# Optimization experiments

Hardware: AMD Instinct MI355X
Metric: run time of the kernel (lower is better)

Reference implementation:

```python
import jax, jax.numpy as jnp
import numpy as np

B, T, V, E, H, C = 128, 200, 50000, 300, 512, 3

def _lstm_scan(x, W_ih, W_hh, b_ih, b_hh, h0, c0):
    # x: [B,T,E]; torch LSTMCell gate order: i, f, g, o
    xg = jnp.einsum('bte,ge->btg', x, W_ih) + b_ih + b_hh  # [B,T,4H]
    def step(carry, xg_t):
        h, c = carry
        gates = xg_t + h @ W_hh.T
        i, f, g, o = jnp.split(gates, 4, axis=-1)
        c = jax.nn.sigmoid(f) * c + jax.nn.sigmoid(i) * jnp.tanh(g)
        h = jax.nn.sigmoid(o) * jnp.tanh(c)
        return (h, c), (h, c)
    _, (hs, cs) = jax.lax.scan(step, (h0, c0), jnp.swapaxes(xg, 0, 1))
    return hs, cs  # [T,B,H]

def _mask_blend(hs, cs, m, h0, c0):
    # hs,cs: [T,B,H]; m: [T,B]; carry-forward previous state where mask==0
    def step(carry, inp):
        h_p, c_p = carry
        h_t, c_t, m_t = inp
        m_t = m_t[:, None]
        h_p = m_t * h_t + (1.0 - m_t) * h_p
        c_p = m_t * c_t + (1.0 - m_t) * c_p
        return (h_p, c_p), (h_p, c_p)
    _, (mh, mc) = jax.lax.scan(step, (h0, c0), (hs, cs, m))
    return mh, mc

def setup_inputs() -> dict:
    key = jax.random.key(0)
    ks = jax.random.split(key, 12)
    s_e = 1.0 / np.sqrt(H)
    u = lambda k, shp: jax.random.uniform(k, shp, jnp.float32, -s_e, s_e)
    return {
        'premise': jax.random.randint(ks[0], (B, T), 0, V),
        'hypothesis': jax.random.randint(ks[1], (B, T), 0, V),
        'similarity': jax.random.uniform(ks[2], (B, 1), jnp.float32),
        'emb_weight': jax.random.normal(ks[3], (V, E), jnp.float32),
        'Wih_p': u(ks[4], (4 * H, E)), 'Whh_p': u(ks[5], (4 * H, H)),
        'bih_p': u(ks[6], (4 * H,)), 'bhh_p': u(ks[7], (4 * H,)),
        'Wih_h': u(ks[8], (4 * H, E)), 'Whh_h': u(ks[9], (4 * H, H)),
        'bih_h': u(ks[10], (4 * H,)), 'bhh_h': u(ks[11], (4 * H,)),
        'fc_W': jax.random.normal(jax.random.fold_in(key, 100), (C, H + 1), jnp.float32) * 0.02,
        'fc_b': jnp.zeros((C,), jnp.float32),
    }

def reference(premise, hypothesis, similarity, emb_weight,
              Wih_p, Whh_p, bih_p, bhh_p, Wih_h, Whh_h, bih_h, bhh_h,
              fc_W, fc_b):
    emb_p = emb_weight[premise]            # [B,T,E]
    emb_h = emb_weight[hypothesis]
    mask_p = (premise != 0).astype(jnp.float32).T   # [T,B]
    mask_h = (hypothesis != 0).astype(jnp.float32).T
    h0 = jnp.zeros((B, H), jnp.float32)
    c0 = jnp.zeros((B, H), jnp.float32)
    # premise LSTM (raw, unmasked recurrence as in original)
    hs_p, cs_p = _lstm_scan(emb_p, Wih_p, Whh_p, bih_p, bhh_p, h0, c0)
    _, mc_p = _mask_blend(hs_p, cs_p, mask_p, h0, c0)
    c_last = mc_p[-1]                      # masked last premise cell
    # hypothesis LSTM: hidden reset, cell carried
    hs_h, cs_h = _lstm_scan(emb_h, Wih_h, Whh_h, bih_h, bhh_h, h0, c_last)
    mh_h, _ = _mask_blend(hs_h, cs_h, mask_h, h0, c_last)
    feat = jnp.concatenate([mh_h[-1], similarity], axis=1)  # [B,H+1]
    logits = feat @ fc_W.T + fc_b
    # dropout inactive (eval mode)
    return jax.nn.log_softmax(logits, axis=1)
```

## Files before the change

kernel.cpp:

```cpp
#include <hip/hip_runtime.h>
#include <hip/hip_bf16.h>

#define B_ 128
#define T_ 200
#define H_ 512
#define G_ 2048
#define E_ 300

typedef unsigned short u16;
typedef unsigned int u32;

using f32x4 = __attribute__((ext_vector_type(4))) float;
using s16x8 = __attribute__((ext_vector_type(8))) short;
using u32x2 = __attribute__((ext_vector_type(2))) u32;

__device__ __forceinline__ u16 f2bf(float f) {
  u32 u = __builtin_bit_cast(u32, f);
  u32 r = (u + 0x7fffu + ((u >> 16) & 1u)) >> 16;
  return (u16)r;
}
__device__ __forceinline__ float bf2f(u16 s) {
  return __builtin_bit_cast(float, (u32)s << 16);
}

__device__ __forceinline__ s16x8 ld_h16_sc(const void* p) {
  s16x8 r;
  asm volatile("global_load_dwordx4 %0, %1, off sc0 sc1" : "=v"(r) : "v"(p));
  return r;
}
__device__ __forceinline__ void st_h_sc(void* p, u32 v) {
  asm volatile("global_store_short %0, %1, off sc0 sc1" :: "v"(p), "v"(v));
}
__device__ __forceinline__ u32 ld_flag_sc(const void* p) {
  u32 r;
  asm volatile("global_load_dword %0, %1, off sc0 sc1\n\ts_waitcnt vmcnt(0)"
               : "=v"(r) : "v"(p) : "memory");
  return r;
}
__device__ __forceinline__ void st_flag_sc(void* p, u32 v) {
  asm volatile("global_store_dword %0, %1, off sc0 sc1" :: "v"(p), "v"(v) : "memory");
}

__global__ __launch_bounds__(256) void wih_cvt(
    const float* __restrict__ W, u16* __restrict__ Wb)
{
  const int idx = blockIdx.x * 256 + threadIdx.x;
  const int row = idx / 320, k = idx - row * 320;
  const float v = (k < E_) ? W[row * E_ + k] : 0.f;
  Wb[idx] = f2bf(v);
}

__global__ __launch_bounds__(64) void mask_k(
    const int* __restrict__ tok, u32* __restrict__ mb)
{
  const int idx = blockIdx.x * 64 + threadIdx.x;
  if (idx >= T_ * 4) return;
  const int t = idx >> 2, w = idx & 3;
  u32 bits = 0;
  for (int i = 0; i < 32; ++i)
    bits |= (tok[(w * 32 + i) * T_ + t] != 0 ? 1u : 0u) << i;
  mb[idx] = bits;
}

__global__ __launch_bounds__(256) void xg_gemm(
    const int* __restrict__ tok, const float* __restrict__ emb,
    const u16* __restrict__ Wb, const float* __restrict__ bih,
    const float* __restrict__ bhh, u16* __restrict__ xg)
{
  __shared__ u16 Al[64 * 320];
  __shared__ u16 Bl[32 * 320];
  __shared__ int tks[64];
  const int tid = threadIdx.x;
  const int bx = blockIdx.x;
  const int m0 = bx * 64;
  if (tid < 64) tks[tid] = tok[((bx & 1) * 64 + tid) * T_ + (bx >> 1)];
  __syncthreads();
  {
    const int row = tid >> 2, part = tid & 3;
    const float* erow = emb + (size_t)tks[row] * E_;
    char* base = (char*)Al + row * 640;
    const int swz = (row & 7) << 4;
#pragma unroll
    for (int i = 0; i < 40; ++i) {
      const int kw = part * 40 + i;
      const int k = kw * 2;
      const float v0 = (k < E_) ? erow[k] : 0.f;
      const float v1 = (k + 1 < E_) ? erow[k + 1] : 0.f;
      *(u32*)(base + ((kw * 4) ^ swz)) = (u32)f2bf(v0) | ((u32)f2bf(v1) << 16);
    }
  }
  __syncthreads();
  const int wv = tid >> 6, ln = tid & 63, lr = ln & 15, lq = ln >> 4;
  const int arow = wv * 16 + lr;
  const char* abase = (const char*)Al + arow * 640;
  const int aswz = (arow & 7) << 4;
  const int brow = tid >> 3, bpart = tid & 7;
  char* bdst = (char*)Bl + brow * 640;
  const int bswz = (brow & 7) << 4;
  const char* b0base = (const char*)Bl + lr * 640;
  const char* b1base = (const char*)Bl + (16 + lr) * 640;
  const int bswz2 = (lr & 7) << 4;

  for (int ni = 0; ni < 8; ++ni) {
    const int n0 = blockIdx.y * 256 + ni * 32;
    {
      const u16* src = Wb + (size_t)(n0 + brow) * 320 + bpart * 40;
#pragma unroll
      for (int i = 0; i < 5; ++i) {
        s16x8 v = *(const s16x8*)(src + i * 8);
        *(s16x8*)(bdst + (((bpart * 5 + i) * 16) ^ bswz)) = v;
      }
    }
    __syncthreads();
    f32x4 acc0 = {0.f, 0.f, 0.f, 0.f}, acc1 = {0.f, 0.f, 0.f, 0.f};
#pragma unroll
    for (int ks = 0; ks < 10; ++ks) {
      const int kb = ks * 64 + lq * 16;
      s16x8 af  = *(const s16x8*)(abase  + (kb ^ aswz));
      s16x8 bf0 = *(const s16x8*)(b0base + (kb ^ bswz2));
      s16x8 bf1 = *(const s16x8*)(b1base + (kb ^ bswz2));
      acc0 = __builtin_amdgcn_mfma_f32_16x16x32_bf16(af, bf0, acc0, 0, 0, 0);
      acc1 = __builtin_amdgcn_mfma_f32_16x16x32_bf16(af, bf1, acc1, 0, 0, 0);
    }
    const int qc = n0 >> 9;
    const int jA = (n0 & 511) + lr;
#pragma unroll
    for (int r = 0; r < 4; ++r) {
      const int m = m0 + wv * 16 + lq * 4 + r;
      const int gA = n0 + lr, gB = n0 + 16 + lr;
      xg[(size_t)m * 2048 + (size_t)jA * 4 + qc]        = f2bf(acc0[r] + bih[gA] + bhh[gA]);
      xg[(size_t)m * 2048 + (size_t)(jA + 16) * 4 + qc] = f2bf(acc1[r] + bih[gB] + bhh[gB]);
    }
    __syncthreads();
  }
}

template<int TRACK_C>
__global__ __launch_bounds__(512, 2) void lstm_rec(
    const u16* __restrict__ xg, const float* __restrict__ Whh,
    u16* __restrict__ hbuf, const float* __restrict__ c0in,
    float* __restrict__ cOut, float* __restrict__ mhOut,
    u32* __restrict__ flags, const u32* __restrict__ maskb)
{
  __shared__ f32x4 red[8][4][64];
  const int tid = threadIdx.x;
  const int wv = tid >> 6, ln = tid & 63, lr = ln & 15, lq = ln >> 4;
  const int grp = (int)blockIdx.x >> 5, jt = (int)blockIdx.x & 31;
  const int j0 = jt * 16, bg0 = grp * 16;
  u32* gflags = flags + grp * 512;

  s16x8 Bf[4][2];
#pragma unroll
  for (int q = 0; q < 4; ++q) {
    const float* wr = Whh + (size_t)(q * H_ + j0 + lr) * H_ + wv * 64 + lq * 8;
#pragma unroll
    for (int ks = 0; ks < 2; ++ks) {
      const float* wp = wr + ks * 32;
      s16x8 f;
#pragma unroll
      for (int i = 0; i < 8; ++i) f[i] = (short)f2bf(wp[i]);
      Bf[q][ks] = f;
    }
  }

  float c[4], mb[4];
#pragma unroll
  for (int r = 0; r < 4; ++r) {
    const int b = bg0 + lq * 4 + r;
    float cv = 0.f;
    if (!TRACK_C && wv == 0) cv = c0in[b * H_ + j0 + lr];
    c[r] = cv;
    mb[r] = TRACK_C ? cv : 0.f;
  }

  const u32* pp = gflags + (ln & 31) * 16;
  const int mword = grp >> 1, mshift = (grp & 1) * 16;

  for (int t = 0; t < T_; ++t) {
    const u16* hrd = hbuf + (t & 1) * (B_ * H_);
    u16* hwr = hbuf + ((t + 1) & 1) * (B_ * H_);

    u32x2 gxp[4];
    u32 mku = 0;
    if (wv == 0) {
      mku = maskb[t * 4 + mword] >> mshift;
#pragma unroll
      for (int r = 0; r < 4; ++r) {
        const int b = bg0 + lq * 4 + r;
        gxp[r] = *(const u32x2*)(xg + (size_t)(t * 128 + b) * 2048
                                    + (size_t)(j0 + lr) * 4);
      }
      if (t > 0) {
        int guard = 0;
        for (;;) {
          u32 v = ld_flag_sc(pp);
          if (__all((int)(v >= (u32)t))) break;
          if (++guard > (1 << 22)) break;
          __builtin_amdgcn_s_sleep(1);
        }
      }
    }
    __syncthreads();
    __builtin_amdgcn_sched_barrier(0);

    s16x8 ha[2];
    const u16* hb = hrd + (size_t)(bg0 + lr) * H_ + wv * 64 + lq * 8;
    ha[0] = ld_h16_sc(hb);
    ha[1] = ld_h16_sc(hb + 32);
    asm volatile("s_waitcnt vmcnt(0)" ::: "memory");
    __builtin_amdgcn_sched_barrier(0);

    f32x4 acc[4];
#pragma unroll
    for (int q = 0; q < 4; ++q) acc[q] = (f32x4){0.f, 0.f, 0.f, 0.f};
#pragma unroll
    for (int ks = 0; ks < 2; ++ks)
#pragma unroll
      for (int q = 0; q < 4; ++q)
        acc[q] = __builtin_amdgcn_mfma_f32_16x16x32_bf16(ha[ks], Bf[q][ks], acc[q], 0, 0, 0);

    if (wv > 0) {
#pragma unroll
      for (int q = 0; q < 4; ++q) red[wv][q][ln] = acc[q];
    }
    __syncthreads();
    if (wv == 0) {
#pragma unroll
      for (int kv = 1; kv < 8; ++kv)
#pragma unroll
        for (int q = 0; q < 4; ++q) acc[q] += red[kv][q][ln];
      const bool last = (t == T_ - 1);
#pragma unroll
      for (int r = 0; r < 4; ++r) {
        const int b = bg0 + lq * 4 + r;
        const u32 lo = gxp[r][0], hi = gxp[r][1];
        const float gi = acc[0][r] + bf2f((u16)lo);
        const float gf = acc[1][r] + bf2f((u16)(lo >> 16));
        const float gG = acc[2][r] + bf2f((u16)hi);
        const float go = acc[3][r] + bf2f((u16)(hi >> 16));
        const float si = 1.f / (1.f + __expf(-gi));
        const float sf = 1.f / (1.f + __expf(-gf));
        const float so = 1.f / (1.f + __expf(-go));
        const float tg = 2.f / (1.f + __expf(-2.f * gG)) - 1.f;
        const float cn = sf * c[r] + si * tg;
        const float tc = 2.f / (1.f + __expf(-2.f * cn)) - 1.f;
        const float hn = so * tc;
        c[r] = cn;
        if ((mku >> (lq * 4 + r)) & 1u) mb[r] = TRACK_C ? cn : hn;
        if (!last) st_h_sc(hwr + (size_t)b * H_ + j0 + lr, (u32)f2bf(hn));
      }
      if (t + 1 < T_) {
        asm volatile("s_waitcnt vmcnt(0)" ::: "memory");
        if (ln == 0) st_flag_sc(gflags + jt * 16, (u32)(t + 1));
      }
    }
    __syncthreads();
  }

  if (wv == 0) {
#pragma unroll
    for (int r = 0; r < 4; ++r) {
      const int b = bg0 + lq * 4 + r;
      if (TRACK_C) cOut[b * H_ + j0 + lr] = mb[r];
      else         mhOut[b * H_ + j0 + lr] = mb[r];
    }
  }
}

__global__ __launch_bounds__(128) void final_k(
    const float* __restrict__ mh, const float* __restrict__ sim,
    const float* __restrict__ fcW, const float* __restrict__ fcb,
    float* __restrict__ out)
{
  const int b = threadIdx.x;
  float l[3];
#pragma unroll
  for (int cc = 0; cc < 3; ++cc) {
    const float* wr = fcW + cc * (H_ + 1);
    float s = fcb[cc] + sim[b] * wr[H_];
    for (int j = 0; j < H_; ++j) s += mh[b * H_ + j] * wr[j];
    l[cc] = s;
  }
  const float m = fmaxf(l[0], fmaxf(l[1], l[2]));
  const float lse = m + logf(__expf(l[0] - m) + __expf(l[1] - m) + __expf(l[2] - m));
  out[b * 3 + 0] = l[0] - lse;
  out[b * 3 + 1] = l[1] - lse;
  out[b * 3 + 2] = l[2] - lse;
}

extern "C" void kernel_launch(void* const* d_in, const int* in_sizes, int n_in,
                              void* d_out, int out_size, void* d_ws, size_t ws_size,
                              hipStream_t stream) {
  const int*   prem = (const int*)d_in[0];
  const int*   hypo = (const int*)d_in[1];
  const float* sim  = (const float*)d_in[2];
  const float* emb  = (const float*)d_in[3];
  const float* WihP = (const float*)d_in[4];
  const float* WhhP = (const float*)d_in[5];
  const float* bihP = (const float*)d_in[6];
  const float* bhhP = (const float*)d_in[7];
  const float* WihH = (const float*)d_in[8];
  const float* WhhH = (const float*)d_in[9];
  const float* bihH = (const float*)d_in[10];
  const float* bhhH = (const float*)d_in[11];
  const float* fcW  = (const float*)d_in[12];
  const float* fcb  = (const float*)d_in[13];
  float* out = (float*)d_out;

  char* ws = (char*)d_ws;
  const size_t XG_BYTES = (size_t)B_ * T_ * G_ * 2;
  const size_t HB_OFF = XG_BYTES;
  const size_t CL_OFF = HB_OFF + (size_t)2 * B_ * H_ * 2;
  const size_t MH_OFF = CL_OFF + (size_t)B_ * H_ * 4;
  const size_t FL_OFF = MH_OFF + (size_t)B_ * H_ * 4;
  const size_t MK_OFF = FL_OFF + 32768;
  const size_t WB_OFF = MK_OFF + 8192;
  const size_t NEED   = WB_OFF + (size_t)G_ * 320 * 2;
  if (ws_size < NEED) return;

  u16*   xg    = (u16*)ws;
  u16*   hbuf  = (u16*)(ws + HB_OFF);
  float* cLast = (float*)(ws + CL_OFF);
  float* mh    = (float*)(ws + MH_OFF);
  u32*   flagsP = (u32*)(ws + FL_OFF);
  u32*   flagsH = flagsP + 4096;
  u32*   maskbP = (u32*)(ws + MK_OFF);
  u32*   maskbH = maskbP + 1024;
  u16*   Wb    = (u16*)(ws + WB_OFF);

  hipMemsetAsync(ws + FL_OFF, 0, 32768, stream);

  dim3 gG(400, 8);
  wih_cvt<<<2560, 256, 0, stream>>>(WihP, Wb);
  mask_k<<<13, 64, 0, stream>>>(prem, maskbP);
  xg_gemm<<<gG, 256, 0, stream>>>(prem, emb, Wb, bihP, bhhP, xg);
  hipMemsetAsync(hbuf, 0, (size_t)B_ * H_ * 2, stream);
  lstm_rec<1><<<256, 512, 0, stream>>>(xg, WhhP, hbuf, nullptr, cLast, nullptr, flagsP, maskbP);
  wih_cvt<<<2560, 256, 0, stream>>>(WihH, Wb);
  mask_k<<<13, 64, 0, stream>>>(hypo, maskbH);
  xg_gemm<<<gG, 256, 0, stream>>>(hypo, emb, Wb, bihH, bhhH, xg);
  hipMemsetAsync(hbuf, 0, (size_t)B_ * H_ * 2, stream);
  lstm_rec<0><<<256, 512, 0, stream>>>(xg, WhhH, hbuf, cLast, nullptr, mh, flagsH, maskbH);
  final_k<<<1, 128, 0, stream>>>(mh, sim, fcW, fcb, out);
}
```

Before: 1.991 ms.

## Replace flag-based inter-block sync with tagged hidden-state words and triple buffering

Removes the per-step global flag barrier between blocks. Each hidden value is now stored as a 32-bit word that packs the bf16 value with a step tag, and consumers poll the h data itself until every tag matches. A triple-buffered h array and a double-buffered LDS reduction allow one __syncthreads per step to be dropped, and the other waves wait on a shared-memory step counter. The trade-off is twice the bytes per h load, extra unpack ALU work, and spin-polling on data that assumes the 32-bit stores are seen atomically.

After: 2.049 ms. 2.9% more time.

```diff
diff --git a/kernel.cpp b/kernel.cpp
--- a/kernel.cpp
+++ b/kernel.cpp
@@ -13,6 +13,7 @@
 using f32x4 = __attribute__((ext_vector_type(4))) float;
 using s16x8 = __attribute__((ext_vector_type(8))) short;
 using u32x2 = __attribute__((ext_vector_type(2))) u32;
+using u32x4 = __attribute__((ext_vector_type(4))) u32;
 
 __device__ __forceinline__ u16 f2bf(float f) {
   u32 u = __builtin_bit_cast(u32, f);
@@ -23,22 +24,13 @@
   return __builtin_bit_cast(float, (u32)s << 16);
 }
 
-__device__ __forceinline__ s16x8 ld_h16_sc(const void* p) {
-  s16x8 r;
+__device__ __forceinline__ u32x4 ld_u32x4_sc(const void* p) {
+  u32x4 r;
   asm volatile("global_load_dwordx4 %0, %1, off sc0 sc1" : "=v"(r) : "v"(p));
   return r;
 }
-__device__ __forceinline__ void st_h_sc(void* p, u32 v) {
-  asm volatile("global_store_short %0, %1, off sc0 sc1" :: "v"(p), "v"(v));
-}
-__device__ __forceinline__ u32 ld_flag_sc(const void* p) {
-  u32 r;
-  asm volatile("global_load_dword %0, %1, off sc0 sc1\n\ts_waitcnt vmcnt(0)"
-               : "=v"(r) : "v"(p) : "memory");
-  return r;
-}
-__device__ __forceinline__ void st_flag_sc(void* p, u32 v) {
-  asm volatile("global_store_dword %0, %1, off sc0 sc1" :: "v"(p), "v"(v) : "memory");
+__device__ __forceinline__ void st_u32_sc(void* p, u32 v) {
+  asm volatile("global_store_dword %0, %1, off sc0 sc1" :: "v"(p), "v"(v));
 }
 
 __global__ __launch_bounds__(256) void wih_cvt(
@@ -138,16 +130,19 @@
 template<int TRACK_C>
 __global__ __launch_bounds__(512, 2) void lstm_rec(
     const u16* __restrict__ xg, const float* __restrict__ Whh,
-    u16* __restrict__ hbuf, const float* __restrict__ c0in,
+    u32* __restrict__ h32, const float* __restrict__ c0in,
     float* __restrict__ cOut, float* __restrict__ mhOut,
-    u32* __restrict__ flags, const u32* __restrict__ maskb)
-{
-  __shared__ f32x4 red[8][4][64];
+    const u32* __restrict__ maskb)
+{
+  __shared__ f32x4 red[2][7][4][64];
+  __shared__ u32 stepS;
   const int tid = threadIdx.x;
   const int wv = tid >> 6, ln = tid & 63, lr = ln & 15, lq = ln >> 4;
   const int grp = (int)blockIdx.x >> 5, jt = (int)blockIdx.x & 31;
   const int j0 = jt * 16, bg0 = grp * 16;
-  u32* gflags = flags + grp * 512;
+  const int BH = B_ * H_;
+  const u32 TAGB = 1u + (TRACK_C ? 0u : 256u);
+  volatile u32* vstep = &stepS;
 
   s16x8 Bf[4][2];
 #pragma unroll
@@ -173,12 +168,21 @@
     mb[r] = TRACK_C ? cv : 0.f;
   }
 
-  const u32* pp = gflags + (ln & 31) * 16;
+  if (wv == 0) {
+#pragma unroll
+    for (int r = 0; r < 4; ++r) {
+      const int b = bg0 + lq * 4 + r;
+      st_u32_sc(h32 + (size_t)b * H_ + j0 + lr, TAGB);
+    }
+  }
+  if (tid == 0) stepS = 0;
+  __syncthreads();
+
   const int mword = grp >> 1, mshift = (grp & 1) * 16;
+  int cur = 0;
 
   for (int t = 0; t < T_; ++t) {
-    const u16* hrd = hbuf + (t & 1) * (B_ * H_);
-    u16* hwr = hbuf + ((t + 1) & 1) * (B_ * H_);
+    const int nxt = (cur == 2) ? 0 : cur + 1;
 
     u32x2 gxp[4];
     u32 mku = 0;
@@ -190,46 +194,67 @@
         gxp[r] = *(const u32x2*)(xg + (size_t)(t * 128 + b) * 2048
                                     + (size_t)(j0 + lr) * 4);
       }
-      if (t > 0) {
-        int guard = 0;
-        for (;;) {
-          u32 v = ld_flag_sc(pp);
-          if (__all((int)(v >= (u32)t))) break;
-          if (++guard > (1 << 22)) break;
-          __builtin_amdgcn_s_sleep(1);
-        }
+    } else {
+      int g0 = 0;
+      while (*vstep < (u32)t) { if (++g0 > (1 << 24)) break; }
+    }
+
+    const u32 tag = TAGB + (u32)t;
+    const u32* hsrc = h32 + (size_t)cur * BH + (size_t)(bg0 + lr) * H_
+                      + wv * 64 + lq * 8;
+    u32x4 hv[4];
+    {
+      int guard = 0;
+      for (;;) {
+        hv[0] = ld_u32x4_sc(hsrc);
+        hv[1] = ld_u32x4_sc(hsrc + 4);
+        hv[2] = ld_u32x4_sc(hsrc + 32);
+        hv[3] = ld_u32x4_sc(hsrc + 36);
+        asm volatile("s_waitcnt vmcnt(0)" ::: "memory");
+        u32 bad = 0;
+#pragma unroll
+        for (int i = 0; i < 4; ++i)
+#pragma unroll
+          for (int e = 0; e < 4; ++e) bad |= (hv[i][e] ^ tag) & 0xFFFFu;
+        if (__all(bad == 0)) break;
+        if (++guard > (1 << 18)) break;
       }
     }
-    __syncthreads();
     __builtin_amdgcn_sched_barrier(0);
 
-    s16x8 ha[2];
-    const u16* hb = hrd + (size_t)(bg0 + lr) * H_ + wv * 64 + lq * 8;
-    ha[0] = ld_h16_sc(hb);
-    ha[1] = ld_h16_sc(hb + 32);
-    asm volatile("s_waitcnt vmcnt(0)" ::: "memory");
-    __builtin_amdgcn_sched_barrier(0);
+    u32x4 w0, w1;
+    w0[0] = (hv[0][0] >> 16) | (hv[0][1] & 0xFFFF0000u);
+    w0[1] = (hv[0][2] >> 16) | (hv[0][3] & 0xFFFF0000u);
+    w0[2] = (hv[1][0] >> 16) | (hv[1][1] & 0xFFFF0000u);
+    w0[3] = (hv[1][2] >> 16) | (hv[1][3] & 0xFFFF0000u);
+    w1[0] = (hv[2][0] >> 16) | (hv[2][1] & 0xFFFF0000u);
+    w1[1] = (hv[2][2] >> 16) | (hv[2][3] & 0xFFFF0000u);
+    w1[2] = (hv[3][0] >> 16) | (hv[3][1] & 0xFFFF0000u);
+    w1[3] = (hv[3][2] >> 16) | (hv[3][3] & 0xFFFF0000u);
+    const s16x8 af0 = __builtin_bit_cast(s16x8, w0);
+    const s16x8 af1 = __builtin_bit_cast(s16x8, w1);
 
     f32x4 acc[4];
 #pragma unroll
-    for (int q = 0; q < 4; ++q) acc[q] = (f32x4){0.f, 0.f, 0.f, 0.f};
-#pragma unroll
-    for (int ks = 0; ks < 2; ++ks)
-#pragma unroll
-      for (int q = 0; q < 4; ++q)
-        acc[q] = __builtin_amdgcn_mfma_f32_16x16x32_bf16(ha[ks], Bf[q][ks], acc[q], 0, 0, 0);
+    for (int q = 0; q < 4; ++q) {
+      acc[q] = __builtin_amdgcn_mfma_f32_16x16x32_bf16(af0, Bf[q][0],
+                   (f32x4){0.f, 0.f, 0.f, 0.f}, 0, 0, 0);
+      acc[q] = __builtin_amdgcn_mfma_f32_16x16x32_bf16(af1, Bf[q][1], acc[q], 0, 0, 0);
+    }
 
     if (wv > 0) {
 #pragma unroll
-      for (int q = 0; q < 4; ++q) red[wv][q][ln] = acc[q];
+      for (int q = 0; q < 4; ++q) red[t & 1][wv - 1][q][ln] = acc[q];
     }
     __syncthreads();
     if (wv == 0) {
 #pragma unroll
       for (int kv = 1; kv < 8; ++kv)
 #pragma unroll
-        for (int q = 0; q < 4; ++q) acc[q] += red[kv][q][ln];
+        for (int q = 0; q < 4; ++q) acc[q] += red[t & 1][kv - 1][q][ln];
       const bool last = (t == T_ - 1);
+      const u32 ntag = TAGB + (u32)(t + 1);
+      u32* hdst = h32 + (size_t)nxt * BH;
 #pragma unroll
       for (int r = 0; r < 4; ++r) {
         const int b = bg0 + lq * 4 + r;
@@ -247,14 +272,13 @@
         const float hn = so * tc;
         c[r] = cn;
         if ((mku >> (lq * 4 + r)) & 1u) mb[r] = TRACK_C ? cn : hn;
-        if (!last) st_h_sc(hwr + (size_t)b * H_ + j0 + lr, (u32)f2bf(hn));
+        if (!last)
+          st_u32_sc(hdst + (size_t)b * H_ + j0 + lr,
+                    ((u32)f2bf(hn) << 16) | ntag);
       }
-      if (t + 1 < T_) {
-        asm volatile("s_waitcnt vmcnt(0)" ::: "memory");
-        if (ln == 0) st_flag_sc(gflags + jt * 16, (u32)(t + 1));
-      }
-    }
-    __syncthreads();
+      if (ln == 0) *vstep = (u32)(t + 1);
+    }
+    cur = nxt;
   }
 
   if (wv == 0) {
@@ -309,37 +333,30 @@
 
   char* ws = (char*)d_ws;
   const size_t XG_BYTES = (size_t)B_ * T_ * G_ * 2;
-  const size_t HB_OFF = XG_BYTES;
-  const size_t CL_OFF = HB_OFF + (size_t)2 * B_ * H_ * 2;
-  const size_t MH_OFF = CL_OFF + (size_t)B_ * H_ * 4;
-  const size_t FL_OFF = MH_OFF + (size_t)B_ * H_ * 4;
-  const size_t MK_OFF = FL_OFF + 32768;
-  const size_t WB_OFF = MK_OFF + 8192;
-  const size_t NEED   = WB_OFF + (size_t)G_ * 320 * 2;
+  const size_t H32_OFF = XG_BYTES;
+  const size_t CL_OFF  = H32_OFF + (size_t)3 * B_ * H_ * 4;
+  const size_t MH_OFF  = CL_OFF + (size_t)B_ * H_ * 4;
+  const size_t MK_OFF  = MH_OFF + (size_t)B_ * H_ * 4;
+  const size_t WB_OFF  = MK_OFF + 8192;
+  const size_t NEED    = WB_OFF + (size_t)G_ * 320 * 2;
   if (ws_size < NEED) return;
 
   u16*   xg    = (u16*)ws;
-  u16*   hbuf  = (u16*)(ws + HB_OFF);
+  u32*   h32   = (u32*)(ws + H32_OFF);
   float* cLast = (float*)(ws + CL_OFF);
   float* mh    = (float*)(ws + MH_OFF);
-  u32*   flagsP = (u32*)(ws + FL_OFF);
-  u32*   flagsH = flagsP + 4096;
   u32*   maskbP = (u32*)(ws + MK_OFF);
   u32*   maskbH = maskbP + 1024;
   u16*   Wb    = (u16*)(ws + WB_OFF);
-
-  hipMemsetAsync(ws + FL_OFF, 0, 32768, stream);
 
   dim3 gG(400, 8);
   wih_cvt<<<2560, 256, 0, stream>>>(WihP, Wb);
   mask_k<<<13, 64, 0, stream>>>(prem, maskbP);
   xg_gemm<<<gG, 256, 0, stream>>>(prem, emb, Wb, bihP, bhhP, xg);
-  hipMemsetAsync(hbuf, 0, (size_t)B_ * H_ * 2, stream);
-  lstm_rec<1><<<256, 512, 0, stream>>>(xg, WhhP, hbuf, nullptr, cLast, nullptr, flagsP, maskbP);
+  lstm_rec<1><<<256, 512, 0, stream>>>(xg, WhhP, h32, nullptr, cLast, nullptr, maskbP);
   wih_cvt<<<2560, 256, 0, stream>>>(WihH, Wb);
   mask_k<<<13, 64, 0, stream>>>(hypo, maskbH);
   xg_gemm<<<gG, 256, 0, stream>>>(hypo, emb, Wb, bihH, bhhH, xg);
-  hipMemsetAsync(hbuf, 0, (size_t)B_ * H_ * 2, stream);
-  lstm_rec<0><<<256, 512, 0, stream>>>(xg, WhhH, hbuf, cLast, nullptr, mh, flagsH, maskbH);
+  lstm_rec<0><<<256, 512, 0, stream>>>(xg, WhhH, h32, cLast, nullptr, mh, maskbH);
   final_k<<<1, 128, 0, stream>>>(mh, sim, fcW, fcb, out);
 }
```

## Interleave two batch groups per recurrent block to hide cross-block sync latency

Applied to the files above, without the earlier changes.

Each recurrent LSTM block now handles two independent 16-row batch groups, interleaved within each timestep, so the grid shrinks from 256 to 128 blocks. While one group waits on its flag barrier, the other group's flags have had time to settle, which is meant to hide the inter-block synchronisation latency that dominates the serial recurrence. Each block also loads its Whh tile only once for both groups. In exchange, each block does twice the MFMA and gate work per step, and wave 0 does all the gate math serially for both halves.

After: 2.919 ms. 46.6% more time.

```diff
diff --git a/kernel.cpp b/kernel.cpp
--- a/kernel.cpp
+++ b/kernel.cpp
@@ -142,12 +142,13 @@
     float* __restrict__ cOut, float* __restrict__ mhOut,
     u32* __restrict__ flags, const u32* __restrict__ maskb)
 {
-  __shared__ f32x4 red[8][4][64];
+  __shared__ f32x4 red[2][7][4][64];
   const int tid = threadIdx.x;
   const int wv = tid >> 6, ln = tid & 63, lr = ln & 15, lq = ln >> 4;
-  const int grp = (int)blockIdx.x >> 5, jt = (int)blockIdx.x & 31;
-  const int j0 = jt * 16, bg0 = grp * 16;
-  u32* gflags = flags + grp * 512;
+  const int pairI = (int)blockIdx.x >> 5, jt = (int)blockIdx.x & 31;
+  const int j0 = jt * 16;
+  const int bg0[2] = { pairI * 16, (pairI + 4) * 16 };
+  u32* gflags = flags + pairI * 1024;
 
   s16x8 Bf[4][2];
 #pragma unroll
@@ -163,107 +164,116 @@
     }
   }
 
-  float c[4], mb[4];
-#pragma unroll
-  for (int r = 0; r < 4; ++r) {
-    const int b = bg0 + lq * 4 + r;
-    float cv = 0.f;
-    if (!TRACK_C && wv == 0) cv = c0in[b * H_ + j0 + lr];
-    c[r] = cv;
-    mb[r] = TRACK_C ? cv : 0.f;
-  }
-
-  const u32* pp = gflags + (ln & 31) * 16;
-  const int mword = grp >> 1, mshift = (grp & 1) * 16;
+  float c[2][4], mb[2][4];
+#pragma unroll
+  for (int ph = 0; ph < 2; ++ph)
+#pragma unroll
+    for (int r = 0; r < 4; ++r) {
+      const int b = bg0[ph] + lq * 4 + r;
+      float cv = 0.f;
+      if (!TRACK_C && wv == 0) cv = c0in[b * H_ + j0 + lr];
+      c[ph][r] = cv;
+      mb[ph][r] = TRACK_C ? cv : 0.f;
+    }
+
+  const u32* pp[2] = { gflags + (ln & 31) * 16,
+                       gflags + 512 + (ln & 31) * 16 };
 
   for (int t = 0; t < T_; ++t) {
     const u16* hrd = hbuf + (t & 1) * (B_ * H_);
     u16* hwr = hbuf + ((t + 1) & 1) * (B_ * H_);
 
-    u32x2 gxp[4];
-    u32 mku = 0;
+    u32x2 gxp[2][4];
+    u32 mku[2];
     if (wv == 0) {
-      mku = maskb[t * 4 + mword] >> mshift;
-#pragma unroll
-      for (int r = 0; r < 4; ++r) {
-        const int b = bg0 + lq * 4 + r;
-        gxp[r] = *(const u32x2*)(xg + (size_t)(t * 128 + b) * 2048
-                                    + (size_t)(j0 + lr) * 4);
-      }
-      if (t > 0) {
+#pragma unroll
+      for (int ph = 0; ph < 2; ++ph) {
+        mku[ph] = maskb[t * 4 + (bg0[ph] >> 5)] >> (bg0[ph] & 31);
+#pragma unroll
+        for (int r = 0; r < 4; ++r) {
+          const int b = bg0[ph] + lq * 4 + r;
+          gxp[ph][r] = *(const u32x2*)(xg + (size_t)(t * 128 + b) * 2048
+                                          + (size_t)(j0 + lr) * 4);
+        }
+      }
+    }
+
+#pragma unroll
+    for (int ph = 0; ph < 2; ++ph) {
+      if (wv == 0 && t > 0) {
         int guard = 0;
         for (;;) {
-          u32 v = ld_flag_sc(pp);
+          u32 v = ld_flag_sc(pp[ph]);
           if (__all((int)(v >= (u32)t))) break;
           if (++guard > (1 << 22)) break;
           __builtin_amdgcn_s_sleep(1);
         }
       }
-    }
-    __syncthreads();
-    __builtin_amdgcn_sched_barrier(0);
-
-    s16x8 ha[2];
-    const u16* hb = hrd + (size_t)(bg0 + lr) * H_ + wv * 64 + lq * 8;
-    ha[0] = ld_h16_sc(hb);
-    ha[1] = ld_h16_sc(hb + 32);
-    asm volatile("s_waitcnt vmcnt(0)" ::: "memory");
-    __builtin_amdgcn_sched_barrier(0);
-
-    f32x4 acc[4];
-#pragma unroll
-    for (int q = 0; q < 4; ++q) acc[q] = (f32x4){0.f, 0.f, 0.f, 0.f};
-#pragma unroll
-    for (int ks = 0; ks < 2; ++ks)
-#pragma unroll
-      for (int q = 0; q < 4; ++q)
-        acc[q] = __builtin_amdgcn_mfma_f32_16x16x32_bf16(ha[ks], Bf[q][ks], acc[q], 0, 0, 0);
-
-    if (wv > 0) {
-#pragma unroll
-      for (int q = 0; q < 4; ++q) red[wv][q][ln] = acc[q];
-    }
-    __syncthreads();
-    if (wv == 0) {
-#pragma unroll
-      for (int kv = 1; kv < 8; ++kv)
-#pragma unroll
-        for (int q = 0; q < 4; ++q) acc[q] += red[kv][q][ln];
-      const bool last = (t == T_ - 1);
+      __syncthreads();
+      __builtin_amdgcn_sched_barrier(0);
+
+      s16x8 ha0, ha1;
+      const u16* hb = hrd + (size_t)(bg0[ph] + lr) * H_ + wv * 64 + lq * 8;
+      ha0 = ld_h16_sc(hb);
+      ha1 = ld_h16_sc(hb + 32);
+      asm volatile("s_waitcnt vmcnt(0)" ::: "memory");
+      __builtin_amdgcn_sched_barrier(0);
+
+      f32x4 acc[4];
+#pragma unroll
+      for (int q = 0; q < 4; ++q) {
+        acc[q] = __builtin_amdgcn_mfma_f32_16x16x32_bf16(ha0, Bf[q][0],
+                     (f32x4){0.f, 0.f, 0.f, 0.f}, 0, 0, 0);
+        acc[q] = __builtin_amdgcn_mfma_f32_16x16x32_bf16(ha1, Bf[q][1], acc[q], 0, 0, 0);
+      }
+
+      if (wv > 0) {
+#pragma unroll
+        for (int q = 0; q < 4; ++q) red[ph][wv - 1][q][ln] = acc[q];
+      }
+      __syncthreads();
+      if (wv == 0) {
+#pragma unroll
+        for (int kv = 1; kv < 8; ++kv)
+#pragma unroll
+          for (int q = 0; q < 4; ++q) acc[q] += red[ph][kv - 1][q][ln];
+        const bool last = (t == T_ - 1);
+#pragma unroll
+        for (int r = 0; r < 4; ++r) {
+          const int b = bg0[ph] + lq * 4 + r;
+          const u32 lo = gxp[ph][r][0], hi = gxp[ph][r][1];
+          const float gi = acc[0][r] + bf2f((u16)lo);
+          const float gf = acc[1][r] + bf2f((u16)(lo >> 16));
+          const float gG = acc[2][r] + bf2f((u16)hi);
+          const float go = acc[3][r] + bf2f((u16)(hi >> 16));
+          const float si = 1.f / (1.f + __expf(-gi));
+          const float sf = 1.f / (1.f + __expf(-gf));
+          const float so = 1.f / (1.f + __expf(-go));
+          const float tg = 2.f / (1.f + __expf(-2.f * gG)) - 1.f;
+          const float cn = sf * c[ph][r] + si * tg;
+          const float tc = 2.f / (1.f + __expf(-2.f * cn)) - 1.f;
+          const float hn = so * tc;
+          c[ph][r] = cn;
+          if ((mku[ph] >> (lq * 4 + r)) & 1u) mb[ph][r] = TRACK_C ? cn : hn;
+          if (!last) st_h_sc(hwr + (size_t)b * H_ + j0 + lr, (u32)f2bf(hn));
+        }
+        if (t + 1 < T_) {
+          asm volatile("s_waitcnt vmcnt(0)" ::: "memory");
+          if (ln == 0) st_flag_sc(gflags + ph * 512 + jt * 16, (u32)(t + 1));
+        }
+      }
+    }
+  }
+
+  if (wv == 0) {
+#pragma unroll
+    for (int ph = 0; ph < 2; ++ph)
 #pragma unroll
       for (int r = 0; r < 4; ++r) {
-        const int b = bg0 + lq * 4 + r;
-        const u32 lo = gxp[r][0], hi = gxp[r][1];
-        const float gi = acc[0][r] + bf2f((u16)lo);
-        const float gf = acc[1][r] + bf2f((u16)(lo >> 16));
-        const float gG = acc[2][r] + bf2f((u16)hi);
-        const float go = acc[3][r] + bf2f((u16)(hi >> 16));
-        const float si = 1.f / (1.f + __expf(-gi));
-        const float sf = 1.f / (1.f + __expf(-gf));
-        const float so = 1.f / (1.f + __expf(-go));
-        const float tg = 2.f / (1.f + __expf(-2.f * gG)) - 1.f;
-        const float cn = sf * c[r] + si * tg;
-        const float tc = 2.f / (1.f + __expf(-2.f * cn)) - 1.f;
-        const float hn = so * tc;
-        c[r] = cn;
-        if ((mku >> (lq * 4 + r)) & 1u) mb[r] = TRACK_C ? cn : hn;
-        if (!last) st_h_sc(hwr + (size_t)b * H_ + j0 + lr, (u32)f2bf(hn));
-      }
-      if (t + 1 < T_) {
-        asm volatile("s_waitcnt vmcnt(0)" ::: "memory");
-        if (ln == 0) st_flag_sc(gflags + jt * 16, (u32)(t + 1));
-      }
-    }
-    __syncthreads();
-  }
-
-  if (wv == 0) {
-#pragma unroll
-    for (int r = 0; r < 4; ++r) {
-      const int b = bg0 + lq * 4 + r;
-      if (TRACK_C) cOut[b * H_ + j0 + lr] = mb[r];
-      else         mhOut[b * H_ + j0 + lr] = mb[r];
-    }
+        const int b = bg0[ph] + lq * 4 + r;
+        if (TRACK_C) cOut[b * H_ + j0 + lr] = mb[ph][r];
+        else         mhOut[b * H_ + j0 + lr] = mb[ph][r];
+      }
   }
 }
 
@@ -335,11 +345,11 @@
   mask_k<<<13, 64, 0, stream>>>(prem, maskbP);
   xg_gemm<<<gG, 256, 0, stream>>>(prem, emb, Wb, bihP, bhhP, xg);
   hipMemsetAsync(hbuf, 0, (size_t)B_ * H_ * 2, stream);
-  lstm_rec<1><<<256, 512, 0, stream>>>(xg, WhhP, hbuf, nullptr, cLast, nullptr, flagsP, maskbP);
+  lstm_rec<1><<<128, 512, 0, stream>>>(xg, WhhP, hbuf, nullptr, cLast, nullptr, flagsP, maskbP);
   wih_cvt<<<2560, 256, 0, stream>>>(WihH, Wb);
   mask_k<<<13, 64, 0, stream>>>(hypo, maskbH);
   xg_gemm<<<gG, 256, 0, stream>>>(hypo, emb, Wb, bihH, bhhH, xg);
   hipMemsetAsync(hbuf, 0, (size_t)B_ * H_ * 2, stream);
-  lstm_rec<0><<<256, 512, 0, stream>>>(xg, WhhH, hbuf, cLast, nullptr, mh, flagsH, maskbH);
+  lstm_rec<0><<<128, 512, 0, stream>>>(xg, WhhH, hbuf, cLast, nullptr, mh, flagsH, maskbH);
   final_k<<<1, 128, 0, stream>>>(mh, sim, fcW, fcb, out);
 }
```
